# Optimization experiments

Measured on AMD Instinct MI355X. Metric: run time of the kernel, lower is better.

The kernel has to match this reference:

```python
import jax, jax.numpy as jnp
import numpy as np
from jax import lax

BS, T, DF = 256, 128, 40
HID, UNITS = 64, 64


def _lstm_seq(x, W, U, b):
    """Keras-style LSTM (gate order i,f,c,o), return_sequences=True, eval mode.
    x: (B,T,Din); W: (Din,4H); U: (H,4H); b: (4H,) -> (B,T,H)."""
    B = x.shape[0]
    H = U.shape[0]
    h0 = jnp.zeros((B, H), x.dtype)
    c0 = jnp.zeros((B, H), x.dtype)

    def step(carry, xt):
        h, c = carry
        z = xt @ W + h @ U + b
        i, f, g, o = jnp.split(z, 4, axis=-1)
        i = jax.nn.sigmoid(i)
        f = jax.nn.sigmoid(f)
        g = jnp.tanh(g)
        o = jax.nn.sigmoid(o)
        c = f * c + i * g
        h = o * jnp.tanh(c)
        return (h, c), h

    _, hs = lax.scan(step, (h0, c0), jnp.swapaxes(x, 0, 1))  # (T,B,H)
    return jnp.swapaxes(hs, 0, 1)


def _norm_abs(a, axis=1):
    aa = jnp.abs(a) + 1e-8
    return aa / jnp.sum(aa, axis=axis, keepdims=True)


def setup_inputs() -> dict:
    key = jax.random.key(0)
    ks = jax.random.split(key, 10)
    s = lambda k, shape, fan: (jax.random.normal(k, shape, jnp.float32) * np.float32(1.0 / np.sqrt(fan)))
    return {
        "x": jax.random.normal(ks[0], (BS, T, DF), jnp.float32),
        "W0": s(ks[1], (DF, 4 * HID), DF),
        "U0": s(ks[2], (HID, 4 * HID), HID),
        "b0": jnp.zeros((4 * HID,), jnp.float32),
        "W1": s(ks[3], (HID, 4 * UNITS), HID),
        "U1": s(ks[4], (UNITS, 4 * UNITS), UNITS),
        "b1": jnp.zeros((4 * UNITS,), jnp.float32),
        "kernel": s(ks[5], (1, 1, DF, UNITS), DF),       # feature projection kernel
        "bias": s(ks[6], (1, 1, DF, UNITS), DF),         # feature projection bias
        "beta_w": s(ks[7], (1, T, 1), T),                # unnormalised time-agg weights
    }


def reference(x, W0, U0, b0, W1, U1, b1, kernel, bias, beta_w):
    # Stacked LSTM encoder (hidden layer + output layer, return_sequences=True)
    h = _lstm_seq(x, W0, U0, b0)                 # (B,T,HID)
    latent_reps = _lstm_seq(h, W1, U1, b1)       # (B,T,UNITS)

    # FeatTimeAttention: per-(b,t) feature projections (activation='linear')
    fp = x[..., None] * kernel + bias            # (B,T,DF,UNITS)

    # OLS alpha estimation: G = X^T X (DF,DF), XTy = X^T y (DF,)
    G = jnp.einsum('btdu,bteu->btde', fp, fp)    # (B,T,DF,DF)
    G_inv = jnp.linalg.inv(G)
    XTy = jnp.einsum('btdu,btu->btd', fp, latent_reps)
    alpha = jnp.einsum('btde,bte->btd', G_inv, XTy)  # (B,T,DF)

    # Approximate latent states and time-weighted aggregation
    o_hat = jnp.einsum('btd,btdu->btu', alpha, fp)   # (B,T,UNITS)
    beta = _norm_abs(beta_w, axis=1)                 # (1,T,1)
    z = jnp.sum(o_hat * beta, axis=1)                # (B,UNITS)
    return z
```

## Files before the change

### kernel.cpp

```cpp
#include <hip/hip_runtime.h>
#include <math.h>

#define DEVI __device__ __forceinline__

DEVI float rlane(float v, int l) {
    return __builtin_bit_cast(float, __builtin_amdgcn_readlane(__builtin_bit_cast(int, v), l));
}
DEVI float sigf(float v) { return 1.0f / (1.0f + __expf(-v)); }
DEVI float tanh_f(float v) {
    v = fminf(fmaxf(v, -15.0f), 15.0f);
    float e = __expf(2.0f * v);
    return (e - 1.0f) / (e + 1.0f);
}

__global__ void precompute_kernel(const float* __restrict__ Kg, const float* __restrict__ Bg,
                                  const float* __restrict__ betaw,
                                  float4* __restrict__ Qg, float4* __restrict__ KBg,
                                  float* __restrict__ beta) {
    int job = blockIdx.x * 256 + threadIdx.x;
    if (job < 1600) {
        int d = job / 40, e = job - d * 40;
        const float* kd = Kg + d * 64;
        const float* ke = Kg + e * 64;
        const float* bd = Bg + d * 64;
        const float* be = Bg + e * 64;
        float kk = 0, kbT = 0, kbr = 0, bb = 0;
        for (int u = 0; u < 64; ++u) {
            kk  = fmaf(kd[u], ke[u], kk);
            kbT = fmaf(ke[u], bd[u], kbT);
            kbr = fmaf(kd[u], be[u], kbr);
            bb  = fmaf(bd[u], be[u], bb);
        }
        Qg[job] = make_float4(kk, kbT, kbr, bb);
    } else if (job < 2880) {
        int j2 = job - 1600;
        int d = j2 >> 5, q = j2 & 31;
        KBg[j2] = make_float4(Kg[d * 64 + 2 * q], Kg[d * 64 + 2 * q + 1],
                              Bg[d * 64 + 2 * q], Bg[d * 64 + 2 * q + 1]);
    }
    if (blockIdx.x == 0) {
        int tid = threadIdx.x;
        __shared__ float red[256];
        float av = (tid < 128) ? (fabsf(betaw[tid]) + 1e-8f) : 0.0f;
        red[tid] = av;
        __syncthreads();
        for (int s = 128; s > 0; s >>= 1) {
            if (tid < s) red[tid] += red[tid + s];
            __syncthreads();
        }
        float tot = red[0];
        if (tid < 128) beta[tid] = av / tot;
    }
}

__global__ __launch_bounds__(512)
void lstm2_kernel(const float* __restrict__ x,
                  const float* __restrict__ W0, const float* __restrict__ U0,
                  const float* __restrict__ b0,
                  const float* __restrict__ W1, const float* __restrict__ U1,
                  const float* __restrict__ b1,
                  float* __restrict__ y) {
    int b = blockIdx.x;
    int tid = threadIdx.x;
    int j = tid & 255;
    int u = tid & 63;
    int lane = tid & 63;
    int grp = __builtin_amdgcn_readfirstlane(tid) >> 8;

    float wcol[64];
    float ucol[64];
    float bj;
    if (grp == 0) {
#pragma unroll
        for (int d = 0; d < 40; ++d) wcol[d] = W0[d * 256 + j];
#pragma unroll
        for (int k = 0; k < 64; ++k) ucol[k] = U0[k * 256 + j];
        bj = b0[j];
    } else {
#pragma unroll
        for (int k = 0; k < 64; ++k) wcol[k] = W1[k * 256 + j];
#pragma unroll
        for (int k = 0; k < 64; ++k) ucol[k] = U1[k * 256 + j];
        bj = b1[j];
    }

    __shared__ float x_lds[128 * 40];
    __shared__ float a_lds[512];
    __shared__ float h1buf[64];
    __shared__ float h2buf[64];
    const float4* xg = (const float4*)(x + (size_t)b * 128 * 40);
    float4* xl = (float4*)x_lds;
    for (int i = tid; i < 128 * 40 / 4; i += 512) xl[i] = xg[i];
    if (tid < 64) { h1buf[tid] = 0.0f; h2buf[tid] = 0.0f; }
    float c1 = 0.0f, c2 = 0.0f;
    __syncthreads();

    int li = (lane < 40) ? lane : 0;
#pragma unroll 1
    for (int s = 0; s <= 128; ++s) {
        float a0 = bj, a1 = 0.0f, a2 = 0.0f, a3 = 0.0f;
        if (grp == 0) {
            if (s < 128) {
                float xv = x_lds[s * 40 + li];
                float hv = h1buf[lane];
#pragma unroll
                for (int d = 0; d < 40; d += 4) {
                    a0 = fmaf(rlane(xv, d), wcol[d], a0);
                    a1 = fmaf(rlane(xv, d + 1), wcol[d + 1], a1);
                    a2 = fmaf(rlane(xv, d + 2), wcol[d + 2], a2);
                    a3 = fmaf(rlane(xv, d + 3), wcol[d + 3], a3);
                }
#pragma unroll
                for (int k = 0; k < 64; k += 4) {
                    a0 = fmaf(rlane(hv, k), ucol[k], a0);
                    a1 = fmaf(rlane(hv, k + 1), ucol[k + 1], a1);
                    a2 = fmaf(rlane(hv, k + 2), ucol[k + 2], a2);
                    a3 = fmaf(rlane(hv, k + 3), ucol[k + 3], a3);
                }
            }
        } else {
            if (s >= 1) {
                float h1x = h1buf[lane];
                float h2v = h2buf[lane];
#pragma unroll
                for (int k = 0; k < 64; k += 4) {
                    a0 = fmaf(rlane(h1x, k), wcol[k], a0);
                    a1 = fmaf(rlane(h1x, k + 1), wcol[k + 1], a1);
                    a2 = fmaf(rlane(h1x, k + 2), wcol[k + 2], a2);
                    a3 = fmaf(rlane(h1x, k + 3), wcol[k + 3], a3);
                }
#pragma unroll
                for (int k = 0; k < 64; k += 4) {
                    a0 = fmaf(rlane(h2v, k), ucol[k], a0);
                    a1 = fmaf(rlane(h2v, k + 1), ucol[k + 1], a1);
                    a2 = fmaf(rlane(h2v, k + 2), ucol[k + 2], a2);
                    a3 = fmaf(rlane(h2v, k + 3), ucol[k + 3], a3);
                }
            }
        }
        float z = (a0 + a1) + (a2 + a3);
        int g = (tid >> 6) & 3;
        float a = (g == 2) ? tanh_f(z) : sigf(z);
        a_lds[tid] = a;
        __syncthreads();
        if (grp == 0) {
            if (tid < 64 && s < 128) {
                float iv = a_lds[u], fv = a_lds[u + 64];
                float gv = a_lds[u + 128], ov = a_lds[u + 192];
                c1 = fmaf(fv, c1, iv * gv);
                h1buf[u] = ov * tanh_f(c1);
            }
        } else {
            if (tid < 320 && s >= 1) {
                float iv = a_lds[256 + u], fv = a_lds[320 + u];
                float gv = a_lds[384 + u], ov = a_lds[448 + u];
                c2 = fmaf(fv, c2, iv * gv);
                float h2 = ov * tanh_f(c2);
                h2buf[u] = h2;
                y[((size_t)b * 128 + (s - 1)) * 64 + u] = h2;
            }
        }
        __syncthreads();
    }
}

__launch_bounds__(256)
__global__ void attn_kernel(const float* __restrict__ xin, const float* __restrict__ yin,
                            const float4* __restrict__ Qg, const float4* __restrict__ KBg,
                            const float* __restrict__ betap, float* __restrict__ zpart) {
    __shared__ float4 sQ4[40 * 41];
    __shared__ float4 sKB4[40 * 33];
    __shared__ float redW[4][64];
    __shared__ float redA[4][64];
    __shared__ float wsf[64];
    __shared__ float asf[64];
    int tid = threadIdx.x;
    for (int i = tid; i < 1600; i += 256) {
        int d = i / 40, e = i - d * 40;
        sQ4[d * 41 + e] = Qg[i];
    }
    for (int i = tid; i < 1280; i += 256) {
        int d = i >> 5, q = i & 31;
        sKB4[d * 33 + q] = KBg[i];
    }
    __syncthreads();

    int b = blockIdx.x >> 2;
    int qq = blockIdx.x & 3;
    int wv = tid >> 6;
    int lane = tid & 63;
    int rl0 = (lane < 40) ? lane : 39;
    const float4* Qrow = sQ4 + rl0 * 41;
    const float4* KBrow = sKB4 + rl0 * 33;

    float2 wsacc = make_float2(0.f, 0.f);
    float2 asacc = make_float2(0.f, 0.f);
    int su = __builtin_amdgcn_readfirstlane(wv);
    int t0u = qq * 32 + su * 8;
    size_t bt0u = (size_t)b * 128 + t0u;

#pragma unroll 1
    for (int it = 0; it < 4; ++it) {
        const float* yr0 = yin + (bt0u + 2 * it) * 64;
        const float* yr1 = yr0 + 64;
        const float* xr0 = xin + (bt0u + 2 * it) * 40;
        const float* xr1 = xr0 + 40;
        float btx = betap[t0u + 2 * it];
        float bty = betap[t0u + 2 * it + 1];

        float2 xv;
        xv.x = xr0[rl0];
        xv.y = xr1[rl0];
        if (lane >= 40) { xv.x = 0.f; xv.y = 0.f; }

        float2 t1a = make_float2(0.f, 0.f), t1b = t1a, t2a = t1a, t2b = t1a;
#pragma unroll
        for (int q = 0; q < 32; ++q) {
            float4 kb = KBrow[q];
            float s0x = yr0[2 * q], s1x = yr0[2 * q + 1];
            float s0y = yr1[2 * q], s1y = yr1[2 * q + 1];
            t1a.x = fmaf(kb.x, s0x, t1a.x); t1a.y = fmaf(kb.x, s0y, t1a.y);
            t1b.x = fmaf(kb.y, s1x, t1b.x); t1b.y = fmaf(kb.y, s1y, t1b.y);
            t2a.x = fmaf(kb.z, s0x, t2a.x); t2a.y = fmaf(kb.z, s0y, t2a.y);
            t2b.x = fmaf(kb.w, s1x, t2b.x); t2b.y = fmaf(kb.w, s1y, t2b.y);
        }

        float2 A[41];
        A[40].x = fmaf(xv.x, t1a.x + t1b.x, t2a.x + t2b.x);
        A[40].y = fmaf(xv.y, t1a.y + t1b.y, t2a.y + t2b.y);
#pragma unroll
        for (int e = 0; e < 40; ++e) {
            float4 q4 = Qrow[e];
            float sxx = xr0[e];
            float sxy = xr1[e];
            A[e].x = fmaf(sxx, fmaf(xv.x, q4.x, q4.y), fmaf(xv.x, q4.z, q4.w));
            A[e].y = fmaf(sxy, fmaf(xv.y, q4.x, q4.y), fmaf(xv.y, q4.z, q4.w));
        }

#pragma unroll
        for (int k = 0; k < 40; ++k) {
            float rpx = __builtin_amdgcn_rcpf(rlane(A[k].x, k));
            float rpy = __builtin_amdgcn_rcpf(rlane(A[k].y, k));
            bool gt = (lane > k);
            float mx = gt ? A[k].x * rpx : 0.f;
            float my = gt ? A[k].y * rpy : 0.f;
#pragma unroll
            for (int jj = k + 1; jj <= 40; ++jj) {
                A[jj].x = fmaf(-mx, rlane(A[jj].x, k), A[jj].x);
                A[jj].y = fmaf(-my, rlane(A[jj].y, k), A[jj].y);
            }
        }

        float2 acc = A[40];
        float2 alpha = make_float2(0.f, 0.f);
#pragma unroll
        for (int k = 39; k >= 0; --k) {
            float xk = rlane(acc.x, k) * __builtin_amdgcn_rcpf(rlane(A[k].x, k));
            float yk = rlane(acc.y, k) * __builtin_amdgcn_rcpf(rlane(A[k].y, k));
            bool eq = (lane == k);
            alpha.x = eq ? xk : alpha.x;
            alpha.y = eq ? yk : alpha.y;
            acc.x = fmaf(-xk, A[k].x, acc.x);
            acc.y = fmaf(-yk, A[k].y, acc.y);
        }

        wsacc.x = fmaf(btx, alpha.x * xv.x, wsacc.x);
        wsacc.y = fmaf(bty, alpha.y * xv.y, wsacc.y);
        asacc.x = fmaf(btx, alpha.x, asacc.x);
        asacc.y = fmaf(bty, alpha.y, asacc.y);
    }

    redW[wv][lane] = wsacc.x + wsacc.y;
    redA[wv][lane] = asacc.x + asacc.y;
    __syncthreads();
    if (tid < 64) {
        wsf[tid] = (redW[0][tid] + redW[1][tid]) + (redW[2][tid] + redW[3][tid]);
    } else if (tid < 128) {
        int d = tid - 64;
        asf[d] = (redA[0][d] + redA[1][d]) + (redA[2][d] + redA[3][d]);
    }
    __syncthreads();
    if (tid < 64) {
        const float* KBf = (const float*)sKB4;
        int u = tid;
        int off = ((u >> 1) << 2) + (u & 1);
        float z = 0.0f;
#pragma unroll
        for (int d = 0; d < 40; ++d) {
            float kv = KBf[d * 132 + off];
            float bv = KBf[d * 132 + off + 2];
            z = fmaf(wsf[d], kv, z);
            z = fmaf(asf[d], bv, z);
        }
        zpart[((size_t)b * 4 + qq) * 64 + u] = z;
    }
}

__global__ void reduce_kernel(const float* __restrict__ zpart, float* __restrict__ out) {
    int idx = blockIdx.x * 256 + threadIdx.x;
    int b = idx >> 6, u = idx & 63;
    const float* zp = zpart + (size_t)b * 4 * 64 + u;
    out[idx] = (zp[0] + zp[64]) + (zp[128] + zp[192]);
}

extern "C" void kernel_launch(void* const* d_in, const int* in_sizes, int n_in,
                              void* d_out, int out_size, void* d_ws, size_t ws_size,
                              hipStream_t stream) {
    const float* x  = (const float*)d_in[0];
    const float* W0 = (const float*)d_in[1];
    const float* U0 = (const float*)d_in[2];
    const float* b0 = (const float*)d_in[3];
    const float* W1 = (const float*)d_in[4];
    const float* U1 = (const float*)d_in[5];
    const float* b1 = (const float*)d_in[6];
    const float* Kg = (const float*)d_in[7];
    const float* Bg = (const float*)d_in[8];
    const float* bw = (const float*)d_in[9];
    float* out = (float*)d_out;

    float* y     = (float*)d_ws;
    float4* Qg   = (float4*)(y + 256 * 128 * 64);
    float4* KBg  = Qg + 1600;
    float* beta  = (float*)(KBg + 1280);
    float* zpart = beta + 128;

    precompute_kernel<<<12, 256, 0, stream>>>(Kg, Bg, bw, Qg, KBg, beta);
    lstm2_kernel<<<256, 512, 0, stream>>>(x, W0, U0, b0, W1, U1, b1, y);
    attn_kernel<<<1024, 256, 0, stream>>>(x, y, Qg, KBg, beta, zpart);
    reduce_kernel<<<64, 256, 0, stream>>>(zpart, out);
}
```

Before: 346.9 us.

## Remove second barrier per LSTM step via double-buffered LDS and redundant cell update

Every wave in each group now recomputes the cell and hidden state redundantly and keeps h in a register, so the recurrent input no longer has to be read back from LDS. The gate and h1 buffers are double-buffered by step parity and the layer-2 pipeline lag grows to two steps, which removes the second __syncthreads per timestep. This trades extra transcendental and ALU work in all waves, plus one more loop iteration, for half the block-wide barriers on the serial critical path.

```diff
diff --git a/kernel.cpp b/kernel.cpp
--- a/kernel.cpp
+++ b/kernel.cpp
@@ -63,7 +63,6 @@
     int b = blockIdx.x;
     int tid = threadIdx.x;
     int j = tid & 255;
-    int u = tid & 63;
     int lane = tid & 63;
     int grp = __builtin_amdgcn_readfirstlane(tid) >> 8;
 
@@ -85,24 +84,24 @@
     }
 
     __shared__ float x_lds[128 * 40];
-    __shared__ float a_lds[512];
-    __shared__ float h1buf[64];
-    __shared__ float h2buf[64];
+    __shared__ float a_lds[2][512];
+    __shared__ float h1buf[2][64];
     const float4* xg = (const float4*)(x + (size_t)b * 128 * 40);
     float4* xl = (float4*)x_lds;
     for (int i = tid; i < 128 * 40 / 4; i += 512) xl[i] = xg[i];
-    if (tid < 64) { h1buf[tid] = 0.0f; h2buf[tid] = 0.0f; }
-    float c1 = 0.0f, c2 = 0.0f;
+    if (tid < 128) h1buf[tid >> 6][tid & 63] = 0.0f;
+    float c = 0.0f;
+    float h = 0.0f;
     __syncthreads();
 
     int li = (lane < 40) ? lane : 0;
 #pragma unroll 1
-    for (int s = 0; s <= 128; ++s) {
+    for (int s = 0; s < 130; ++s) {
+        int p = s & 1;
         float a0 = bj, a1 = 0.0f, a2 = 0.0f, a3 = 0.0f;
         if (grp == 0) {
             if (s < 128) {
                 float xv = x_lds[s * 40 + li];
-                float hv = h1buf[lane];
 #pragma unroll
                 for (int d = 0; d < 40; d += 4) {
                     a0 = fmaf(rlane(xv, d), wcol[d], a0);
@@ -112,16 +111,15 @@
                 }
 #pragma unroll
                 for (int k = 0; k < 64; k += 4) {
-                    a0 = fmaf(rlane(hv, k), ucol[k], a0);
-                    a1 = fmaf(rlane(hv, k + 1), ucol[k + 1], a1);
-                    a2 = fmaf(rlane(hv, k + 2), ucol[k + 2], a2);
-                    a3 = fmaf(rlane(hv, k + 3), ucol[k + 3], a3);
+                    a0 = fmaf(rlane(h, k), ucol[k], a0);
+                    a1 = fmaf(rlane(h, k + 1), ucol[k + 1], a1);
+                    a2 = fmaf(rlane(h, k + 2), ucol[k + 2], a2);
+                    a3 = fmaf(rlane(h, k + 3), ucol[k + 3], a3);
                 }
             }
         } else {
-            if (s >= 1) {
-                float h1x = h1buf[lane];
-                float h2v = h2buf[lane];
+            if (s >= 2) {
+                float h1x = h1buf[p][lane];
 #pragma unroll
                 for (int k = 0; k < 64; k += 4) {
                     a0 = fmaf(rlane(h1x, k), wcol[k], a0);
@@ -131,36 +129,37 @@
                 }
 #pragma unroll
                 for (int k = 0; k < 64; k += 4) {
-                    a0 = fmaf(rlane(h2v, k), ucol[k], a0);
-                    a1 = fmaf(rlane(h2v, k + 1), ucol[k + 1], a1);
-                    a2 = fmaf(rlane(h2v, k + 2), ucol[k + 2], a2);
-                    a3 = fmaf(rlane(h2v, k + 3), ucol[k + 3], a3);
+                    a0 = fmaf(rlane(h, k), ucol[k], a0);
+                    a1 = fmaf(rlane(h, k + 1), ucol[k + 1], a1);
+                    a2 = fmaf(rlane(h, k + 2), ucol[k + 2], a2);
+                    a3 = fmaf(rlane(h, k + 3), ucol[k + 3], a3);
                 }
             }
         }
         float z = (a0 + a1) + (a2 + a3);
         int g = (tid >> 6) & 3;
         float a = (g == 2) ? tanh_f(z) : sigf(z);
-        a_lds[tid] = a;
+        a_lds[p][tid] = a;
         __syncthreads();
         if (grp == 0) {
-            if (tid < 64 && s < 128) {
-                float iv = a_lds[u], fv = a_lds[u + 64];
-                float gv = a_lds[u + 128], ov = a_lds[u + 192];
-                c1 = fmaf(fv, c1, iv * gv);
-                h1buf[u] = ov * tanh_f(c1);
+            if (s < 128) {
+                const float* pp = &a_lds[p][0];
+                float iv = pp[lane], fv = pp[lane + 64];
+                float gv = pp[lane + 128], ov = pp[lane + 192];
+                c = fmaf(fv, c, iv * gv);
+                h = ov * tanh_f(c);
+                if (tid < 64) h1buf[p][lane] = h;
             }
         } else {
-            if (tid < 320 && s >= 1) {
-                float iv = a_lds[256 + u], fv = a_lds[320 + u];
-                float gv = a_lds[384 + u], ov = a_lds[448 + u];
-                c2 = fmaf(fv, c2, iv * gv);
-                float h2 = ov * tanh_f(c2);
-                h2buf[u] = h2;
-                y[((size_t)b * 128 + (s - 1)) * 64 + u] = h2;
-            }
-        }
-        __syncthreads();
+            if (s >= 2) {
+                const float* pp = &a_lds[p][256];
+                float iv = pp[lane], fv = pp[lane + 64];
+                float gv = pp[lane + 128], ov = pp[lane + 192];
+                c = fmaf(fv, c, iv * gv);
+                h = ov * tanh_f(c);
+                if (tid < 320) y[((size_t)b * 128 + (s - 2)) * 64 + lane] = h;
+            }
+        }
     }
 }
 
```

Measured after the change: 348.8 us. Within noise of the previous version (+0.5%).
